# Performance work log

Hardware: AMD Instinct MI355X
Metric: run time of the kernel (lower is better)

The kernel has to match this reference:

```python
import jax, jax.numpy as jnp
import numpy as np

N_NODES = 100_000
N_EDGES = 1_600_000
NUM_GRAPHS = 16_384
F_IN = 4      # PLAYER_FEATURES
HID = 32      # HIDDEN_DIM


def setup_inputs() -> dict:
    key = jax.random.key(0)
    ks = jax.random.split(key, 12)
    x = jax.random.normal(ks[0], (N_NODES, F_IN), jnp.float32)
    edge_index = jax.random.randint(ks[1], (2, N_EDGES), 0, N_NODES, dtype=jnp.int32)
    edge_weight = jax.random.uniform(ks[2], (N_EDGES,), jnp.float32)
    batch = jnp.sort(jax.random.randint(ks[3], (N_NODES,), 0, NUM_GRAPHS, dtype=jnp.int32))
    # GCNConv weights (glorot-ish scale) and biases
    W1 = jax.random.normal(ks[4], (F_IN, HID), jnp.float32) / np.sqrt(F_IN)
    b1 = jnp.zeros((HID,), jnp.float32)
    W2 = jax.random.normal(ks[5], (HID, HID), jnp.float32) / np.sqrt(HID)
    b2 = jnp.zeros((HID,), jnp.float32)
    Wo = jax.random.normal(ks[6], (HID, 1), jnp.float32) / np.sqrt(HID)
    bo = jnp.zeros((1,), jnp.float32)
    Wb = jax.random.normal(ks[7], (HID, 1), jnp.float32) / np.sqrt(HID)
    bb = jnp.zeros((1,), jnp.float32)
    return {"x": x, "edge_index": edge_index, "edge_weight": edge_weight,
            "batch": batch, "num_graphs": NUM_GRAPHS,
            "W1": W1, "b1": b1, "W2": W2, "b2": b2,
            "Wo": Wo, "bo": bo, "Wb": Wb, "bb": bb}


def _gcn_conv(x, src, dst, w, W, b, n):
    # PyG GCNConv: symmetric normalization with self-loops already in (src,dst,w)
    deg = jax.ops.segment_sum(w, dst, num_segments=n)                 # weighted degree [n]
    dinv = jnp.where(deg > 0, jax.lax.rsqrt(deg), 0.0)
    norm = dinv[src] * w * dinv[dst]                                  # [E+n]
    h = x @ W                                                         # transform first
    agg = jax.ops.segment_sum(h[src] * norm[:, None], dst, num_segments=n)
    return agg + b


def reference(x, edge_index, edge_weight, batch, num_graphs,
              W1, b1, W2, b2, Wo, bo, Wb, bb):
    n = x.shape[0]
    loop = jnp.arange(n, dtype=edge_index.dtype)
    src = jnp.concatenate([edge_index[0], loop])   # add self-loops (fill weight 1)
    dst = jnp.concatenate([edge_index[1], loop])
    w = jnp.concatenate([edge_weight, jnp.ones((n,), edge_weight.dtype)])

    h = jax.nn.relu(_gcn_conv(x, src, dst, w, W1, b1, n))
    h = jax.nn.relu(_gcn_conv(h, src, dst, w, W2, b2, n))

    # global_mean_pool over batch assignment
    sums = jax.ops.segment_sum(h, batch, num_segments=num_graphs)
    cnt = jax.ops.segment_sum(jnp.ones((n,), h.dtype), batch, num_segments=num_graphs)
    pooled = sums / jnp.maximum(cnt, 1.0)[:, None]                    # [G, HID]

    orange = jax.nn.sigmoid(pooled @ Wo + bo)                          # [G, 1]
    blue = jax.nn.sigmoid(pooled @ Wb + bb)                            # [G, 1]
    return (orange, blue)
```

## Files before the change

### kernel.cpp

```cpp
#include <hip/hip_runtime.h>
#include <math.h>

#define FIN 4
#define HID 32
#define EPB 4096
#define BUCK_SH 9
#define BUCK_W 512
#define NBUCK_MAX 256
#define CAP 12288

__device__ __forceinline__ unsigned pack_bf16x2(float a, float b) {
    unsigned ua = __float_as_uint(a); ua += 0x7FFF + ((ua >> 16) & 1);
    unsigned ub = __float_as_uint(b); ub += 0x7FFF + ((ub >> 16) & 1);
    return (ua >> 16) | (ub & 0xFFFF0000u);
}
__device__ __forceinline__ float bf_lo(unsigned u) { return __uint_as_float(u << 16); }
__device__ __forceinline__ float bf_hi(unsigned u) { return __uint_as_float(u & 0xFFFF0000u); }
__device__ __forceinline__ float dec_w(unsigned u) { return ((float)(u >> 17) + 0.5f) * (1.0f / 32768.0f); }

__global__ void p1a_bounds(const int* __restrict__ dst, const int* __restrict__ batch,
                           int* __restrict__ counts, int* __restrict__ gstart,
                           int E, int n, int nbuck, int G) {
    __shared__ int h[NBUCK_MAX];
    int t = threadIdx.x;
    for (int q = t; q < nbuck; q += 256) h[q] = 0;
    __syncthreads();
    int base = blockIdx.x * EPB;
    for (int k = t; k < EPB; k += 256) {
        int e = base + k;
        if (e < E) atomicAdd(&h[dst[e] >> BUCK_SH], 1);
    }
    __syncthreads();
    for (int q = t; q < nbuck; q += 256) counts[blockIdx.x * nbuck + q] = h[q];
    int i = blockIdx.x * 256 + t;
    if (i < n) {
        int b = batch[i];
        if (i == 0) {
            for (int g = 0; g <= b; ++g) gstart[g] = 0;
        } else {
            int p = batch[i - 1];
            for (int g = p + 1; g <= b; ++g) gstart[g] = i;
        }
        if (i == n - 1) {
            for (int g = b + 1; g <= G; ++g) gstart[g] = n;
        }
    }
}

__global__ void rowscan_kernel(const int* __restrict__ counts, int* __restrict__ offsets,
                               int* __restrict__ bucketCnt, int nblk, int nbuck) {
    __shared__ int s[512];
    int b = blockIdx.x;
    int t = threadIdx.x;
    int v = (t < nblk) ? counts[t * nbuck + b] : 0;
    s[t] = v;
    __syncthreads();
    for (int off = 1; off < 512; off <<= 1) {
        int u = (t >= off) ? s[t - off] : 0;
        __syncthreads();
        s[t] += u;
        __syncthreads();
    }
    if (t < nblk) offsets[t * nbuck + b] = b * CAP + s[t] - v;
    if (t == nblk - 1) bucketCnt[b] = s[t];
}

__global__ void p1c_scatter(const int* __restrict__ src, const int* __restrict__ dst,
                            const float* __restrict__ w, const int* __restrict__ offsets,
                            unsigned long long* __restrict__ bkt, int E, int nbuck) {
    __shared__ int cur[NBUCK_MAX];
    int t = threadIdx.x;
    for (int q = t; q < nbuck; q += 256) cur[q] = offsets[blockIdx.x * nbuck + q];
    __syncthreads();
    int base = blockIdx.x * EPB;
    for (int k = t; k < EPB; k += 256) {
        int e = base + k;
        if (e < E) {
            int d = dst[e];
            int sN = src[e];
            float wv = w[e];
            unsigned wfix = (unsigned)(wv * 32768.0f);
            wfix = wfix > 32767u ? 32767u : wfix;
            int b = d >> BUCK_SH;
            int pos = atomicAdd(&cur[b], 1);
            unsigned hi = ((unsigned)(d & (BUCK_W - 1)) << 17) | (unsigned)sN;
            bkt[pos] = ((unsigned long long)hi << 32) | wfix;
        }
    }
}

__global__ void p2_csr(const unsigned long long* __restrict__ bkt, const int* __restrict__ bucketCnt,
                       const float* __restrict__ x, unsigned* __restrict__ csr4,
                       int* __restrict__ rowptr, int* __restrict__ cntv,
                       float* __restrict__ dinv, float* __restrict__ xs, int n) {
    __shared__ int lcnt[BUCK_W];
    __shared__ int s[BUCK_W];
    __shared__ int curL[BUCK_W];
    __shared__ int wsumI[BUCK_W];
    int b = blockIdx.x;
    int t = threadIdx.x;
    int base = b * CAP;
    int cnt  = bucketCnt[b];
    lcnt[t] = 0;
    wsumI[t] = 0;
    __syncthreads();
    for (int k = t; k < cnt; k += BUCK_W) {
        unsigned hi = (unsigned)(bkt[base + k] >> 32);
        atomicAdd(&lcnt[hi >> 17], 1);
    }
    __syncthreads();
    s[t] = lcnt[t];
    __syncthreads();
    for (int off = 1; off < BUCK_W; off <<= 1) {
        int v = (t >= off) ? s[t - off] : 0;
        __syncthreads();
        s[t] += v;
        __syncthreads();
    }
    int excl = s[t] - lcnt[t];
    curL[t] = excl;
    int node = (b << BUCK_SH) + t;
    if (node < n) { rowptr[node] = base + excl; cntv[node] = lcnt[t]; }
    __syncthreads();
    for (int k = t; k < cnt; k += BUCK_W) {
        unsigned long long v = bkt[base + k];
        unsigned hi = (unsigned)(v >> 32);
        unsigned wfix = (unsigned)v;
        int ld = hi >> 17;
        int sN = hi & 0x1FFFF;
        int p = atomicAdd(&curL[ld], 1);
        csr4[base + p] = (wfix << 17) | (unsigned)sN;
        atomicAdd(&wsumI[ld], (int)wfix);
    }
    __syncthreads();
    if (node < n) {
        float wsum = ((float)wsumI[t] + 0.5f * (float)lcnt[t]) * (1.0f / 32768.0f);
        float di = rsqrtf(wsum + 1.0f);
        dinv[node] = di;
        float4 xv = *reinterpret_cast<const float4*>(x + (size_t)node * FIN);
        xv.x *= di; xv.y *= di; xv.z *= di; xv.w *= di;
        *reinterpret_cast<float4*>(xs + (size_t)node * FIN) = xv;
    }
}

__global__ void layer1_kernel(const float* __restrict__ xs, const int* __restrict__ rowptr,
                              const int* __restrict__ cntv, const unsigned* __restrict__ csr4,
                              const float* __restrict__ dinv, const float* __restrict__ W1,
                              const float* __restrict__ b1, unsigned* __restrict__ h1, int n) {
    __shared__ float sW[FIN * HID];
    __shared__ float sb[HID];
    int t = threadIdx.x;
    if (t < FIN * HID) sW[t] = W1[t];
    if (t < HID) sb[t] = b1[t];
    __syncthreads();
    int i = blockIdx.x * blockDim.x + t;
    if (i >= n) return;
    float di = dinv[i];
    float4 a = *reinterpret_cast<const float4*>(xs + (size_t)i * FIN);
    int beg = rowptr[i], c = cntv[i];
    int j = 0;
    for (; j + 3 < c; j += 4) {
        unsigned u0 = __builtin_nontemporal_load(csr4 + beg + j);
        unsigned u1 = __builtin_nontemporal_load(csr4 + beg + j + 1);
        unsigned u2 = __builtin_nontemporal_load(csr4 + beg + j + 2);
        unsigned u3 = __builtin_nontemporal_load(csr4 + beg + j + 3);
        float4 v0 = *reinterpret_cast<const float4*>(xs + (size_t)(u0 & 0x1FFFF) * FIN);
        float4 v1 = *reinterpret_cast<const float4*>(xs + (size_t)(u1 & 0x1FFFF) * FIN);
        float4 v2 = *reinterpret_cast<const float4*>(xs + (size_t)(u2 & 0x1FFFF) * FIN);
        float4 v3 = *reinterpret_cast<const float4*>(xs + (size_t)(u3 & 0x1FFFF) * FIN);
        float w0 = dec_w(u0), w1 = dec_w(u1), w2 = dec_w(u2), w3 = dec_w(u3);
        a.x += w0*v0.x + w1*v1.x + w2*v2.x + w3*v3.x;
        a.y += w0*v0.y + w1*v1.y + w2*v2.y + w3*v3.y;
        a.z += w0*v0.z + w1*v1.z + w2*v2.z + w3*v3.z;
        a.w += w0*v0.w + w1*v1.w + w2*v2.w + w3*v3.w;
    }
    for (; j < c; ++j) {
        unsigned u0 = __builtin_nontemporal_load(csr4 + beg + j);
        float w0 = dec_w(u0);
        float4 v0 = *reinterpret_cast<const float4*>(xs + (size_t)(u0 & 0x1FFFF) * FIN);
        a.x += w0*v0.x; a.y += w0*v0.y; a.z += w0*v0.z; a.w += w0*v0.w;
    }
    a.x *= di; a.y *= di; a.z *= di; a.w *= di;
    unsigned pk[16];
    #pragma unroll
    for (int k = 0; k < HID; k += 2) {
        float h0 = fmaxf(sb[k]   + a.x*sW[0*HID+k]   + a.y*sW[1*HID+k]   + a.z*sW[2*HID+k]   + a.w*sW[3*HID+k],   0.f);
        float h1v= fmaxf(sb[k+1] + a.x*sW[0*HID+k+1] + a.y*sW[1*HID+k+1] + a.z*sW[2*HID+k+1] + a.w*sW[3*HID+k+1], 0.f);
        pk[k / 2] = pack_bf16x2(di * h0, di * h1v);
    }
    uint4* hp = reinterpret_cast<uint4*>(h1 + (size_t)i * 16);
    hp[0] = make_uint4(pk[0], pk[1], pk[2], pk[3]);
    hp[1] = make_uint4(pk[4], pk[5], pk[6], pk[7]);
    hp[2] = make_uint4(pk[8], pk[9], pk[10], pk[11]);
    hp[3] = make_uint4(pk[12], pk[13], pk[14], pk[15]);
}

__global__ __launch_bounds__(256) void layer2_kernel(
        const unsigned* __restrict__ h1, const int* __restrict__ rowptr,
        const int* __restrict__ cntv, const unsigned* __restrict__ csr4,
        const float* __restrict__ dinv, const float* __restrict__ W2,
        const float* __restrict__ b2, unsigned* __restrict__ h2, int n) {
    __shared__ float sW[HID * HID];
    __shared__ float sb[HID];
    __shared__ float sAgg[32][HID + 1];
    int t = threadIdx.x;
    for (int q = t; q < HID * HID; q += 256) sW[q] = W2[q];
    if (t < HID) sb[t] = b2[t];
    __syncthreads();
    int nib = t >> 3;
    int l   = t & 7;
    int i = blockIdx.x * 32 + nib;
    const uint2* h1d = reinterpret_cast<const uint2*>(h1);
    float a0, a1, a2, a3;
    if (i < n) {
        uint2 hv = h1d[(size_t)i * 8 + l];
        a0 = bf_lo(hv.x);
        a1 = bf_hi(hv.x);
        a2 = bf_lo(hv.y);
        a3 = bf_hi(hv.y);
        int beg = rowptr[i], c = cntv[i];
        int j = 0;
        for (; j + 3 < c; j += 4) {
            unsigned u0 = __builtin_nontemporal_load(csr4 + beg + j);
            unsigned u1 = __builtin_nontemporal_load(csr4 + beg + j + 1);
            unsigned u2 = __builtin_nontemporal_load(csr4 + beg + j + 2);
            unsigned u3 = __builtin_nontemporal_load(csr4 + beg + j + 3);
            uint2 s0 = h1d[(size_t)(u0 & 0x1FFFF) * 8 + l];
            uint2 s1 = h1d[(size_t)(u1 & 0x1FFFF) * 8 + l];
            uint2 s2 = h1d[(size_t)(u2 & 0x1FFFF) * 8 + l];
            uint2 s3 = h1d[(size_t)(u3 & 0x1FFFF) * 8 + l];
            float w0 = dec_w(u0), w1 = dec_w(u1), w2 = dec_w(u2), w3 = dec_w(u3);
            a0 += w0 * bf_lo(s0.x);
            a1 += w0 * bf_hi(s0.x);
            a2 += w0 * bf_lo(s0.y);
            a3 += w0 * bf_hi(s0.y);
            a0 += w1 * bf_lo(s1.x);
            a1 += w1 * bf_hi(s1.x);
            a2 += w1 * bf_lo(s1.y);
            a3 += w1 * bf_hi(s1.y);
            a0 += w2 * bf_lo(s2.x);
            a1 += w2 * bf_hi(s2.x);
            a2 += w2 * bf_lo(s2.y);
            a3 += w2 * bf_hi(s2.y);
            a0 += w3 * bf_lo(s3.x);
            a1 += w3 * bf_hi(s3.x);
            a2 += w3 * bf_lo(s3.y);
            a3 += w3 * bf_hi(s3.y);
        }
        for (; j < c; ++j) {
            unsigned u0 = __builtin_nontemporal_load(csr4 + beg + j);
            float w0 = dec_w(u0);
            uint2 s0 = h1d[(size_t)(u0 & 0x1FFFF) * 8 + l];
            a0 += w0 * bf_lo(s0.x);
            a1 += w0 * bf_hi(s0.x);
            a2 += w0 * bf_lo(s0.y);
            a3 += w0 * bf_hi(s0.y);
        }
        float di = dinv[i];
        a0 *= di; a1 *= di; a2 *= di; a3 *= di;
    } else {
        a0 = a1 = a2 = a3 = 0.f;
    }
    sAgg[nib][l * 4 + 0] = a0;
    sAgg[nib][l * 4 + 1] = a1;
    sAgg[nib][l * 4 + 2] = a2;
    sAgg[nib][l * 4 + 3] = a3;
    __syncthreads();
    if (i < n) {
        int k0 = l * 4;
        float o0 = sb[k0], o1 = sb[k0 + 1], o2 = sb[k0 + 2], o3 = sb[k0 + 3];
        #pragma unroll
        for (int j2 = 0; j2 < HID; ++j2) {
            float av = sAgg[nib][j2];
            o0 += av * sW[j2 * HID + k0];
            o1 += av * sW[j2 * HID + k0 + 1];
            o2 += av * sW[j2 * HID + k0 + 2];
            o3 += av * sW[j2 * HID + k0 + 3];
        }
        uint2 pkd;
        pkd.x = pack_bf16x2(fmaxf(o0, 0.f), fmaxf(o1, 0.f));
        pkd.y = pack_bf16x2(fmaxf(o2, 0.f), fmaxf(o3, 0.f));
        reinterpret_cast<uint2*>(h2)[(size_t)i * 8 + l] = pkd;
    }
}

__global__ void poolheads_kernel(const unsigned* __restrict__ h2, const int* __restrict__ gstart,
                                 const float* __restrict__ Wo, const float* __restrict__ bo,
                                 const float* __restrict__ Wb, const float* __restrict__ bb,
                                 float* __restrict__ out, int G) {
    int g = blockIdx.x * 4 + (threadIdx.x >> 6);
    int lane = threadIdx.x & 63;
    int k = lane & 31;
    int half = lane >> 5;
    if (g >= G) return;
    int s0 = gstart[g], s1 = gstart[g + 1];
    float sum = 0.f;
    const unsigned short* h2s = reinterpret_cast<const unsigned short*>(h2);
    for (int i = s0 + half; i < s1; i += 2) {
        unsigned u = (unsigned)h2s[(size_t)i * HID + k] << 16;
        sum += __uint_as_float(u);
    }
    float cnt = (float)(s1 - s0);
    float inv = 1.0f / fmaxf(cnt, 1.0f);
    float m = sum * inv;
    float po = m * Wo[k];
    float pb = m * Wb[k];
    #pragma unroll
    for (int off = 32; off >= 1; off >>= 1) {
        po += __shfl_xor(po, off);
        pb += __shfl_xor(pb, off);
    }
    if (lane == 0) {
        out[g]     = 1.0f / (1.0f + expf(-(po + bo[0])));
        out[G + g] = 1.0f / (1.0f + expf(-(pb + bb[0])));
    }
}

extern "C" void kernel_launch(void* const* d_in, const int* in_sizes, int n_in,
                              void* d_out, int out_size, void* d_ws, size_t ws_size,
                              hipStream_t stream) {
    const float* x     = (const float*)d_in[0];
    const int*   ei    = (const int*)d_in[1];
    const float* ew    = (const float*)d_in[2];
    const int*   batch = (const int*)d_in[3];
    const float* W1 = (const float*)d_in[5];
    const float* b1 = (const float*)d_in[6];
    const float* W2 = (const float*)d_in[7];
    const float* b2 = (const float*)d_in[8];
    const float* Wo = (const float*)d_in[9];
    const float* bo = (const float*)d_in[10];
    const float* Wb = (const float*)d_in[11];
    const float* bb = (const float*)d_in[12];
    float* out = (float*)d_out;

    const int n = in_sizes[0] / FIN;
    const int E = in_sizes[2];
    const int G = out_size / 2;
    const int* src = ei;
    const int* dst = ei + E;
    const int n4 = (n + 3) & ~3;
    const int nblk  = (E + EPB - 1) / EPB;
    const int nbuck = (n + BUCK_W - 1) / BUCK_W;
    const int M  = nblk * nbuck;
    const int Mp = (M + 3) & ~3;

    char* wsb = (char*)d_ws;
    unsigned long long* bkt = (unsigned long long*)wsb;
    unsigned* csr4     = (unsigned*)(wsb + (size_t)nbuck * CAP * 8);
    int*      counts   = (int*)(csr4 + (size_t)nbuck * CAP);
    int*      offsets  = counts + Mp;
    int*      bucketCnt= offsets + Mp;
    int*      rowptr   = bucketCnt + 256;
    int*      cntv     = rowptr + n4;
    float*    dinv     = (float*)(cntv + n4);
    float*    xs       = dinv + n4;
    int*      gstart   = (int*)(xs + (size_t)n4 * FIN);
    unsigned* h1       = (unsigned*)(gstart + G + 16);
    unsigned* h2       = h1 + (size_t)n4 * 16;

    const int B = 256;
    p1a_bounds   <<<nblk, 256, 0, stream>>>(dst, batch, counts, gstart, E, n, nbuck, G);
    rowscan_kernel<<<nbuck, 512, 0, stream>>>(counts, offsets, bucketCnt, nblk, nbuck);
    p1c_scatter  <<<nblk, 256, 0, stream>>>(src, dst, ew, offsets, bkt, E, nbuck);
    p2_csr       <<<nbuck, BUCK_W, 0, stream>>>(bkt, bucketCnt, x, csr4, rowptr, cntv, dinv, xs, n);
    layer1_kernel<<<(n + B - 1) / B, B, 0, stream>>>(xs, rowptr, cntv, csr4, dinv, W1, b1, h1, n);
    layer2_kernel<<<(n + 31) / 32, B, 0, stream>>>(h1, rowptr, cntv, csr4, dinv, W2, b2, h2, n);
    poolheads_kernel<<<(G + 3) / 4, B, 0, stream>>>(h2, gstart, Wo, bo, Wb, bb, out, G);
}
```

Measured before the change: 110.3 us.

## Privatize bucket histograms per wave, widen CSR build block, deepen gather unroll

The bucket-count histogram in p1a_bounds is split into four per-wavefront copies that are summed at the end, which lowers shared-memory atomic contention. p2_csr now runs with 1024 threads per bucket, and the weighted-degree atomics move into the first counting pass. That leaves the scatter pass with a single atomic per edge, at the cost of idle threads during the scan. Both aggregation kernels add an 8-wide unrolled gather loop so more independent loads are in flight, which raises register pressure.

Result: faster. 105.4 us, median of 2 (-4.4%).

```diff
diff --git a/kernel.cpp b/kernel.cpp
--- a/kernel.cpp
+++ b/kernel.cpp
@@ -21,17 +21,19 @@
 __global__ void p1a_bounds(const int* __restrict__ dst, const int* __restrict__ batch,
                            int* __restrict__ counts, int* __restrict__ gstart,
                            int E, int n, int nbuck, int G) {
-    __shared__ int h[NBUCK_MAX];
-    int t = threadIdx.x;
-    for (int q = t; q < nbuck; q += 256) h[q] = 0;
+    __shared__ int h[4][NBUCK_MAX];
+    int t = threadIdx.x;
+    int wv = t >> 6;
+    for (int q = t; q < 4 * NBUCK_MAX; q += 256) ((int*)h)[q] = 0;
     __syncthreads();
     int base = blockIdx.x * EPB;
     for (int k = t; k < EPB; k += 256) {
         int e = base + k;
-        if (e < E) atomicAdd(&h[dst[e] >> BUCK_SH], 1);
-    }
-    __syncthreads();
-    for (int q = t; q < nbuck; q += 256) counts[blockIdx.x * nbuck + q] = h[q];
+        if (e < E) atomicAdd(&h[wv][dst[e] >> BUCK_SH], 1);
+    }
+    __syncthreads();
+    for (int q = t; q < nbuck; q += 256)
+        counts[blockIdx.x * nbuck + q] = h[0][q] + h[1][q] + h[2][q] + h[3][q];
     int i = blockIdx.x * 256 + t;
     if (i < n) {
         int b = batch[i];
@@ -89,10 +91,11 @@
     }
 }
 
-__global__ void p2_csr(const unsigned long long* __restrict__ bkt, const int* __restrict__ bucketCnt,
-                       const float* __restrict__ x, unsigned* __restrict__ csr4,
-                       int* __restrict__ rowptr, int* __restrict__ cntv,
-                       float* __restrict__ dinv, float* __restrict__ xs, int n) {
+__global__ __launch_bounds__(1024) void p2_csr(
+        const unsigned long long* __restrict__ bkt, const int* __restrict__ bucketCnt,
+        const float* __restrict__ x, unsigned* __restrict__ csr4,
+        int* __restrict__ rowptr, int* __restrict__ cntv,
+        float* __restrict__ dinv, float* __restrict__ xs, int n) {
     __shared__ int lcnt[BUCK_W];
     __shared__ int s[BUCK_W];
     __shared__ int curL[BUCK_W];
@@ -101,28 +104,31 @@
     int t = threadIdx.x;
     int base = b * CAP;
     int cnt  = bucketCnt[b];
-    lcnt[t] = 0;
-    wsumI[t] = 0;
-    __syncthreads();
-    for (int k = t; k < cnt; k += BUCK_W) {
-        unsigned hi = (unsigned)(bkt[base + k] >> 32);
+    if (t < BUCK_W) { lcnt[t] = 0; wsumI[t] = 0; }
+    __syncthreads();
+    for (int k = t; k < cnt; k += 1024) {
+        unsigned long long v = bkt[base + k];
+        unsigned hi = (unsigned)(v >> 32);
         atomicAdd(&lcnt[hi >> 17], 1);
-    }
-    __syncthreads();
-    s[t] = lcnt[t];
+        atomicAdd(&wsumI[hi >> 17], (int)(unsigned)v);
+    }
+    __syncthreads();
+    if (t < BUCK_W) s[t] = lcnt[t];
     __syncthreads();
     for (int off = 1; off < BUCK_W; off <<= 1) {
-        int v = (t >= off) ? s[t - off] : 0;
+        int v = (t < BUCK_W && t >= off) ? s[t - off] : 0;
         __syncthreads();
-        s[t] += v;
+        if (t < BUCK_W) s[t] += v;
         __syncthreads();
     }
-    int excl = s[t] - lcnt[t];
-    curL[t] = excl;
     int node = (b << BUCK_SH) + t;
-    if (node < n) { rowptr[node] = base + excl; cntv[node] = lcnt[t]; }
-    __syncthreads();
-    for (int k = t; k < cnt; k += BUCK_W) {
+    if (t < BUCK_W) {
+        int excl = s[t] - lcnt[t];
+        curL[t] = excl;
+        if (node < n) { rowptr[node] = base + excl; cntv[node] = lcnt[t]; }
+    }
+    __syncthreads();
+    for (int k = t; k < cnt; k += 1024) {
         unsigned long long v = bkt[base + k];
         unsigned hi = (unsigned)(v >> 32);
         unsigned wfix = (unsigned)v;
@@ -130,10 +136,9 @@
         int sN = hi & 0x1FFFF;
         int p = atomicAdd(&curL[ld], 1);
         csr4[base + p] = (wfix << 17) | (unsigned)sN;
-        atomicAdd(&wsumI[ld], (int)wfix);
-    }
-    __syncthreads();
-    if (node < n) {
+    }
+    __syncthreads();
+    if (t < BUCK_W && node < n) {
         float wsum = ((float)wsumI[t] + 0.5f * (float)lcnt[t]) * (1.0f / 32768.0f);
         float di = rsqrtf(wsum + 1.0f);
         dinv[node] = di;
@@ -159,20 +164,31 @@
     float4 a = *reinterpret_cast<const float4*>(xs + (size_t)i * FIN);
     int beg = rowptr[i], c = cntv[i];
     int j = 0;
+    for (; j + 7 < c; j += 8) {
+        unsigned u[8];
+        float4 v[8];
+        #pragma unroll
+        for (int q = 0; q < 8; ++q) u[q] = __builtin_nontemporal_load(csr4 + beg + j + q);
+        #pragma unroll
+        for (int q = 0; q < 8; ++q) v[q] = *reinterpret_cast<const float4*>(xs + (size_t)(u[q] & 0x1FFFF) * FIN);
+        #pragma unroll
+        for (int q = 0; q < 8; ++q) {
+            float wq = dec_w(u[q]);
+            a.x += wq * v[q].x; a.y += wq * v[q].y; a.z += wq * v[q].z; a.w += wq * v[q].w;
+        }
+    }
     for (; j + 3 < c; j += 4) {
-        unsigned u0 = __builtin_nontemporal_load(csr4 + beg + j);
-        unsigned u1 = __builtin_nontemporal_load(csr4 + beg + j + 1);
-        unsigned u2 = __builtin_nontemporal_load(csr4 + beg + j + 2);
-        unsigned u3 = __builtin_nontemporal_load(csr4 + beg + j + 3);
-        float4 v0 = *reinterpret_cast<const float4*>(xs + (size_t)(u0 & 0x1FFFF) * FIN);
-        float4 v1 = *reinterpret_cast<const float4*>(xs + (size_t)(u1 & 0x1FFFF) * FIN);
-        float4 v2 = *reinterpret_cast<const float4*>(xs + (size_t)(u2 & 0x1FFFF) * FIN);
-        float4 v3 = *reinterpret_cast<const float4*>(xs + (size_t)(u3 & 0x1FFFF) * FIN);
-        float w0 = dec_w(u0), w1 = dec_w(u1), w2 = dec_w(u2), w3 = dec_w(u3);
-        a.x += w0*v0.x + w1*v1.x + w2*v2.x + w3*v3.x;
-        a.y += w0*v0.y + w1*v1.y + w2*v2.y + w3*v3.y;
-        a.z += w0*v0.z + w1*v1.z + w2*v2.z + w3*v3.z;
-        a.w += w0*v0.w + w1*v1.w + w2*v2.w + w3*v3.w;
+        unsigned u[4];
+        float4 v[4];
+        #pragma unroll
+        for (int q = 0; q < 4; ++q) u[q] = __builtin_nontemporal_load(csr4 + beg + j + q);
+        #pragma unroll
+        for (int q = 0; q < 4; ++q) v[q] = *reinterpret_cast<const float4*>(xs + (size_t)(u[q] & 0x1FFFF) * FIN);
+        #pragma unroll
+        for (int q = 0; q < 4; ++q) {
+            float wq = dec_w(u[q]);
+            a.x += wq * v[q].x; a.y += wq * v[q].y; a.z += wq * v[q].z; a.w += wq * v[q].w;
+        }
     }
     for (; j < c; ++j) {
         unsigned u0 = __builtin_nontemporal_load(csr4 + beg + j);
@@ -220,32 +236,37 @@
         a3 = bf_hi(hv.y);
         int beg = rowptr[i], c = cntv[i];
         int j = 0;
+        for (; j + 7 < c; j += 8) {
+            unsigned u[8];
+            uint2 sv[8];
+            #pragma unroll
+            for (int q = 0; q < 8; ++q) u[q] = __builtin_nontemporal_load(csr4 + beg + j + q);
+            #pragma unroll
+            for (int q = 0; q < 8; ++q) sv[q] = h1d[(size_t)(u[q] & 0x1FFFF) * 8 + l];
+            #pragma unroll
+            for (int q = 0; q < 8; ++q) {
+                float wq = dec_w(u[q]);
+                a0 += wq * bf_lo(sv[q].x);
+                a1 += wq * bf_hi(sv[q].x);
+                a2 += wq * bf_lo(sv[q].y);
+                a3 += wq * bf_hi(sv[q].y);
+            }
+        }
         for (; j + 3 < c; j += 4) {
-            unsigned u0 = __builtin_nontemporal_load(csr4 + beg + j);
-            unsigned u1 = __builtin_nontemporal_load(csr4 + beg + j + 1);
-            unsigned u2 = __builtin_nontemporal_load(csr4 + beg + j + 2);
-            unsigned u3 = __builtin_nontemporal_load(csr4 + beg + j + 3);
-            uint2 s0 = h1d[(size_t)(u0 & 0x1FFFF) * 8 + l];
-            uint2 s1 = h1d[(size_t)(u1 & 0x1FFFF) * 8 + l];
-            uint2 s2 = h1d[(size_t)(u2 & 0x1FFFF) * 8 + l];
-            uint2 s3 = h1d[(size_t)(u3 & 0x1FFFF) * 8 + l];
-            float w0 = dec_w(u0), w1 = dec_w(u1), w2 = dec_w(u2), w3 = dec_w(u3);
-            a0 += w0 * bf_lo(s0.x);
-            a1 += w0 * bf_hi(s0.x);
-            a2 += w0 * bf_lo(s0.y);
-            a3 += w0 * bf_hi(s0.y);
-            a0 += w1 * bf_lo(s1.x);
-            a1 += w1 * bf_hi(s1.x);
-            a2 += w1 * bf_lo(s1.y);
-            a3 += w1 * bf_hi(s1.y);
-            a0 += w2 * bf_lo(s2.x);
-            a1 += w2 * bf_hi(s2.x);
-            a2 += w2 * bf_lo(s2.y);
-            a3 += w2 * bf_hi(s2.y);
-            a0 += w3 * bf_lo(s3.x);
-            a1 += w3 * bf_hi(s3.x);
-            a2 += w3 * bf_lo(s3.y);
-            a3 += w3 * bf_hi(s3.y);
+            unsigned u[4];
+            uint2 sv[4];
+            #pragma unroll
+            for (int q = 0; q < 4; ++q) u[q] = __builtin_nontemporal_load(csr4 + beg + j + q);
+            #pragma unroll
+            for (int q = 0; q < 4; ++q) sv[q] = h1d[(size_t)(u[q] & 0x1FFFF) * 8 + l];
+            #pragma unroll
+            for (int q = 0; q < 4; ++q) {
+                float wq = dec_w(u[q]);
+                a0 += wq * bf_lo(sv[q].x);
+                a1 += wq * bf_hi(sv[q].x);
+                a2 += wq * bf_lo(sv[q].y);
+                a3 += wq * bf_hi(sv[q].y);
+            }
         }
         for (; j < c; ++j) {
             unsigned u0 = __builtin_nontemporal_load(csr4 + beg + j);
@@ -362,7 +383,7 @@
     p1a_bounds   <<<nblk, 256, 0, stream>>>(dst, batch, counts, gstart, E, n, nbuck, G);
     rowscan_kernel<<<nbuck, 512, 0, stream>>>(counts, offsets, bucketCnt, nblk, nbuck);
     p1c_scatter  <<<nblk, 256, 0, stream>>>(src, dst, ew, offsets, bkt, E, nbuck);
-    p2_csr       <<<nbuck, BUCK_W, 0, stream>>>(bkt, bucketCnt, x, csr4, rowptr, cntv, dinv, xs, n);
+    p2_csr       <<<nbuck, 1024, 0, stream>>>(bkt, bucketCnt, x, csr4, rowptr, cntv, dinv, xs, n);
     layer1_kernel<<<(n + B - 1) / B, B, 0, stream>>>(xs, rowptr, cntv, csr4, dinv, W1, b1, h1, n);
     layer2_kernel<<<(n + 31) / 32, B, 0, stream>>>(h1, rowptr, cntv, csr4, dinv, W2, b2, h2, n);
     poolheads_kernel<<<(G + 3) / 4, B, 0, stream>>>(h2, gstart, Wo, bo, Wb, bb, out, G);
```
